# Kernel optimization log

Measured on AMD Instinct MI355X. Metric: run time of the kernel, lower is better.

Reference implementation:

```python
import jax, jax.numpy as jnp
import numpy as np

B, S, E, H = 2, 2048, 1024, 16
D = E // H  # head_dim = 64


def setup_inputs() -> dict:
    key = jax.random.key(0)
    ks = jax.random.split(key, 8)
    s = 0.02
    return {
        "queries": jax.random.normal(ks[0], (B, S, E), jnp.float32),
        "keys": jax.random.normal(ks[1], (B, S, E), jnp.float32),
        "values": jax.random.normal(ks[2], (B, S, E), jnp.float32),
        "mask": jnp.ones((B, 1, 1, S), jnp.int32),
        "Wq": jax.random.normal(ks[3], (E, E), jnp.float32) * s,
        "bq": jnp.zeros((E,), jnp.float32),
        "Wk": jax.random.normal(ks[4], (E, E), jnp.float32) * s,
        "bk": jnp.zeros((E,), jnp.float32),
        "Wv": jax.random.normal(ks[5], (E, E), jnp.float32) * s,
        "bv": jnp.zeros((E,), jnp.float32),
        "Wo": jax.random.normal(ks[6], (E, E), jnp.float32) * s,
        "bo": jnp.zeros((E,), jnp.float32),
    }


def reference(queries, keys, values, mask, Wq, bq, Wk, bk, Wv, bv, Wo, bo):
    # NOTE: faithful to source, W_v is applied to the `keys` input; `values` is unused.
    q = queries @ Wq.T + bq            # [B,S,E]
    k = keys @ Wk.T + bk               # [B,S,E]
    v = keys @ Wv.T + bv               # [B,S,E]
    q = q.reshape(B, S, H, D)
    k = k.reshape(B, S, H, D)
    v = v.reshape(B, S, H, D)
    scale = 1.0 / jnp.sqrt(jnp.asarray(D, q.dtype))
    scores = jnp.einsum("nqhd,nkhd->nhqk", q, k)   # [B,H,S,S] full score matrix
    scores = jnp.where(mask == 0, jnp.asarray(-1e20, scores.dtype), scores)
    attn = jax.nn.softmax(scores * scale, axis=-1)
    out = jnp.einsum("nhqk,nkhd->nqhd", attn, v).reshape(B, S, E)
    return out @ Wo.T + bo
```

## Files before the change

### kernel.cpp

```cpp
#include <hip/hip_runtime.h>
#include <hip/hip_bf16.h>
#include <stdint.h>

#define NB 2
#define NS 2048
#define NE 1024
#define NH 16
#define ND 64

typedef __attribute__((ext_vector_type(4))) float f32x4;
typedef __attribute__((ext_vector_type(16))) float f32x16;
typedef __attribute__((ext_vector_type(8))) short s16x8;
typedef __attribute__((ext_vector_type(4))) unsigned short u16x4;
typedef __attribute__((ext_vector_type(2))) unsigned int uint2v;

__device__ __forceinline__ unsigned short f2bf(float f) {
  union { float f; unsigned int i; } u; u.f = f;
  unsigned int r = u.i + 0x7FFFu + ((u.i >> 16) & 1u);
  return (unsigned short)(r >> 16);
}

__device__ __forceinline__ unsigned cvtpk_bf16(float lo, float hi) {
  unsigned r;
  asm("v_cvt_pk_bf16_f32 %0, %1, %2" : "=v"(r) : "v"(lo), "v"(hi));
  return r;
}

__device__ __forceinline__ void gload_lds16(const void* g, void* l) {
  __builtin_amdgcn_global_load_lds(
      (const __attribute__((address_space(1))) uint32_t*)g,
      (__attribute__((address_space(3))) uint32_t*)l, 16, 0, 0);
}

__device__ __forceinline__ f32x4 mfma16(s16x8 a, s16x8 b, f32x4 c) {
  return __builtin_amdgcn_mfma_f32_16x16x32_bf16(a, b, c, 0, 0, 0);
}
__device__ __forceinline__ f32x16 mfma32(s16x8 a, s16x8 b, f32x16 c) {
  return __builtin_amdgcn_mfma_f32_32x32x16_bf16(a, b, c, 0, 0, 0);
}

__global__ void conv_x2(const float* __restrict__ a, const float* __restrict__ b,
                        unsigned short* __restrict__ da, unsigned short* __restrict__ db,
                        int n4) {
  const float* s = blockIdx.y ? b : a;
  unsigned short* d = blockIdx.y ? db : da;
  int i = blockIdx.x * blockDim.x + threadIdx.x;
  int stride = gridDim.x * blockDim.x;
  for (; i < n4; i += stride) {
    float4 v = ((const float4*)s)[i];
    u16x4 o;
    o.x = f2bf(v.x); o.y = f2bf(v.y); o.z = f2bf(v.z); o.w = f2bf(v.w);
    ((u16x4*)d)[i] = o;
  }
}

__global__ void conv_w4(const float* __restrict__ s0, const float* __restrict__ s1,
                        const float* __restrict__ s2, const float* __restrict__ s3,
                        unsigned short* __restrict__ d0, unsigned short* __restrict__ d1,
                        unsigned short* __restrict__ d2, unsigned short* __restrict__ d3,
                        int n4) {
  const float* s; unsigned short* d;
  switch (blockIdx.y) {
    case 0: s = s0; d = d0; break;
    case 1: s = s1; d = d1; break;
    case 2: s = s2; d = d2; break;
    default: s = s3; d = d3; break;
  }
  int i = blockIdx.x * blockDim.x + threadIdx.x;
  int stride = gridDim.x * blockDim.x;
  for (; i < n4; i += stride) {
    float4 v = ((const float4*)s)[i];
    u16x4 o;
    o.x = f2bf(v.x); o.y = f2bf(v.y); o.z = f2bf(v.z); o.w = f2bf(v.w);
    ((u16x4*)d)[i] = o;
  }
}

template <int EPI>
__global__ __launch_bounds__(256, 2) void gemm_bt(
    const unsigned short* __restrict__ A,
    const unsigned short* __restrict__ W0, const unsigned short* __restrict__ W1,
    const float* __restrict__ b0, const float* __restrict__ b1,
    void* __restrict__ out0, void* __restrict__ out1) {
  constexpr int BM = 64;
  constexpr int K = 1024;
  __shared__ char smem[2 * (BM * 128 + 16384)];
  const int t = threadIdx.x;
  const int lane = t & 63;
  const int wv = t >> 6;
  const int wr = wv >> 1, wc = wv & 1;
  const int bm = blockIdx.y * BM, bn = blockIdx.x * 128;
  const int lr = lane & 15, lg = lane >> 4;

  const unsigned short* Wp = W0;
  const float* bp = b0;
  int nloc = bn;
  if constexpr (EPI == 3) {
    if (bn >= 1024) { Wp = W1; bp = b1; nloc = bn - 1024; }
  }

  f32x4 acc[2][4] = {};

  auto stage = [&](int buf, int k0) {
    char* As = smem + buf * (BM * 128 + 16384);
    char* Bs = As + BM * 128;
#pragma unroll
    for (int r = 0; r < BM / 32; ++r) {
      int lin = r * 256 + t;
      int row = lin >> 3;
      int scb = ((lin & 7) << 4) ^ ((row & 7) << 4);
      gload_lds16((const char*)(A + (size_t)(bm + row) * K + k0) + scb,
                  As + (size_t)(r * 256 + (t & ~63)) * 16);
    }
#pragma unroll
    for (int r = 0; r < 4; ++r) {
      int lin = r * 256 + t;
      int row = lin >> 3;
      int scb = ((lin & 7) << 4) ^ ((row & 7) << 4);
      gload_lds16((const char*)(Wp + (size_t)(nloc + row) * K + k0) + scb,
                  Bs + (size_t)(r * 256 + (t & ~63)) * 16);
    }
  };

  stage(0, 0);
  for (int t6 = 0; t6 < K / 64; ++t6) {
    const int cur = t6 & 1;
    if (t6 + 1 < K / 64) {
      stage(cur ^ 1, (t6 + 1) * 64);
      asm volatile("s_waitcnt vmcnt(6)" ::: "memory");
    } else {
      asm volatile("s_waitcnt vmcnt(0)" ::: "memory");
    }
    asm volatile("s_barrier" ::: "memory");

    const char* As = smem + cur * (BM * 128 + 16384);
    const char* Bs = As + BM * 128;
    s16x8 af[2][2], bfr[4][2];
#pragma unroll
    for (int mf = 0; mf < 2; ++mf)
#pragma unroll
      for (int kk = 0; kk < 2; ++kk) {
        int row = wr * 32 + mf * 16 + lr;
        int cb = (lg << 4) + (kk << 6);
        af[mf][kk] = *(const s16x8*)(As + row * 128 + (cb ^ ((row & 7) << 4)));
      }
#pragma unroll
    for (int nf = 0; nf < 4; ++nf)
#pragma unroll
      for (int kk = 0; kk < 2; ++kk) {
        int row = wc * 64 + nf * 16 + lr;
        int cb = (lg << 4) + (kk << 6);
        bfr[nf][kk] = *(const s16x8*)(Bs + row * 128 + (cb ^ ((row & 7) << 4)));
      }
#pragma unroll
    for (int mf = 0; mf < 2; ++mf)
#pragma unroll
      for (int nf = 0; nf < 4; ++nf)
#pragma unroll
        for (int kk = 0; kk < 2; ++kk)
          acc[mf][nf] = mfma16(af[mf][kk], bfr[nf][kk], acc[mf][nf]);

    asm volatile("s_waitcnt lgkmcnt(0)" ::: "memory");
    asm volatile("s_barrier" ::: "memory");
  }

#pragma unroll
  for (int mf = 0; mf < 2; ++mf)
#pragma unroll
    for (int nf = 0; nf < 4; ++nf) {
      int m0 = bm + wr * 32 + mf * 16 + (lg << 2);
      int nc = wc * 64 + nf * 16 + lr;
      int n = bn + nc;
      float bv = bp[nloc + nc];
      if constexpr (EPI == 0) {
        unsigned short* C = (unsigned short*)out0;
#pragma unroll
        for (int r = 0; r < 4; ++r)
          C[(size_t)(m0 + r) * 1024 + n] = f2bf(acc[mf][nf][r] + bv);
      } else if constexpr (EPI == 2) {
        float* C = (float*)out0;
#pragma unroll
        for (int r = 0; r < 4; ++r)
          C[(size_t)(m0 + r) * 1024 + n] = acc[mf][nf][r] + bv;
      } else {
        if (n < 1024) {
          unsigned short* C = (unsigned short*)out0;
#pragma unroll
          for (int r = 0; r < 4; ++r)
            C[(size_t)(m0 + r) * 1024 + n] = f2bf(acc[mf][nf][r] + bv);
        } else {
          unsigned short* C = (unsigned short*)out1;
          int nv = n - 1024;
          int b = m0 >> 11, s = m0 & 2047;
          u16x4 o;
          o.x = f2bf(acc[mf][nf][0] + bv);
          o.y = f2bf(acc[mf][nf][1] + bv);
          o.z = f2bf(acc[mf][nf][2] + bv);
          o.w = f2bf(acc[mf][nf][3] + bv);
          *(u16x4*)&C[((size_t)b * NE + nv) * NS + s] = o;
        }
      }
    }
}

__global__ __launch_bounds__(256, 2) void attn_fwd(
    const unsigned short* __restrict__ qb, const unsigned short* __restrict__ kb,
    const unsigned short* __restrict__ vt, const int* __restrict__ mask,
    unsigned short* __restrict__ ob) {
  __shared__ char smem[32768];
  const int t = threadIdx.x, lane = t & 63, wv = t >> 6;
  const int l31 = lane & 31, hi = lane >> 5;
  const int sw = (l31 & 15) << 4;
  const int bh = blockIdx.y, b = bh >> 4, h = bh & 15;
  const int q = blockIdx.x * 128 + wv * 32 + l31;
  const float C = 0.18033688f;

  s16x8 qf[4];
#pragma unroll
  for (int ks = 0; ks < 4; ++ks)
    qf[ks] = *(const s16x8*)&qb[((size_t)(b * NS + q)) * NE + h * ND + ks * 16 + hi * 8];

  f32x16 oacc[2] = {};
  float m = -1e30f, l = 0.f;

  auto stage = [&](int buf, int kt) {
    char* Ks = smem + buf * 16384;
    char* Vs = Ks + 8192;
#pragma unroll
    for (int r = 0; r < 2; ++r) {
      int L = (r * 256 + t) * 16;
      int row = L >> 8;
      int offp = (L & 255) ^ ((row & 15) << 4);
      int key = row + ((offp >> 7) << 5);
      int dby = offp & 127;
      gload_lds16((const char*)&kb[((size_t)(b * NS + kt + key)) * NE + h * ND] + dby,
                  Ks + (r * 256 + (t & ~63)) * 16);
    }
#pragma unroll
    for (int r = 0; r < 2; ++r) {
      int L = (r * 256 + t) * 16;
      int row = L >> 8;
      int offp = (L & 255) ^ ((row & 15) << 4);
      int d = row + ((offp >> 7) << 5);
      int kby = offp & 127;
      gload_lds16((const char*)&vt[((size_t)((b * NH + h) * ND + d)) * NS + kt] + kby,
                  Vs + (r * 256 + (t & ~63)) * 16);
    }
  };

  stage(0, 0);
  asm volatile("s_waitcnt vmcnt(0)" ::: "memory");
  __syncthreads();

  for (int kt = 0; kt < NS; kt += 64) {
    const int cur = (kt >> 6) & 1;
    if (kt + 64 < NS) stage(cur ^ 1, kt + 64);
    const char* Ks = smem + cur * 16384;
    const char* Vs = Ks + 8192;

    int mk = mask[b * NS + kt + lane];

    f32x16 st[2] = {};
    __builtin_amdgcn_s_setprio(1);
#pragma unroll
    for (int t2 = 0; t2 < 2; ++t2)
#pragma unroll
      for (int ks = 0; ks < 4; ++ks) {
        s16x8 kf = *(const s16x8*)(Ks + l31 * 256 +
                                   ((t2 * 128 + ks * 32 + hi * 16) ^ sw));
        st[t2] = mfma32(kf, qf[ks], st[t2]);
      }
    __builtin_amdgcn_s_setprio(0);

    float tm[16];
#pragma unroll
    for (int r = 0; r < 16; ++r) tm[r] = fmaxf(st[0][r], st[1][r]);
    float a0 = fmaxf(fmaxf(tm[0], tm[1]), tm[2]);
    float a1 = fmaxf(fmaxf(tm[3], tm[4]), tm[5]);
    float a2 = fmaxf(fmaxf(tm[6], tm[7]), tm[8]);
    float a3 = fmaxf(fmaxf(tm[9], tm[10]), tm[11]);
    float a4 = fmaxf(fmaxf(tm[12], tm[13]), tm[14]);
    float b0 = fmaxf(fmaxf(a0, a1), a2);
    float b1 = fmaxf(fmaxf(a3, a4), tm[15]);
    float mxl = fmaxf(b0, b1);
    float mx = fmaxf(mxl, __shfl_xor(mxl, 32));

    if (!__all(mx - m <= 44.0f)) {
      float mnew = fmaxf(m, mx);
      float corr = __builtin_amdgcn_exp2f((m - mnew) * C);
#pragma unroll
      for (int td = 0; td < 2; ++td)
#pragma unroll
        for (int r = 0; r < 16; ++r) oacc[td][r] *= corr;
      l *= corr;
      m = mnew;
    }
    const float mC = m * C;

#pragma unroll
    for (int t2 = 0; t2 < 2; ++t2)
#pragma unroll
      for (int r = 0; r < 16; ++r)
        st[t2][r] = __builtin_amdgcn_exp2f(__builtin_fmaf(st[t2][r], C, -mC));

    unsigned long long bal = __ballot(mk != 0);
    if (bal != ~0ull) {
#pragma unroll
      for (int t2 = 0; t2 < 2; ++t2)
#pragma unroll
        for (int r = 0; r < 16; ++r) {
          int key = t2 * 32 + (r & 3) + 8 * (r >> 2) + 4 * hi;
          if (!((bal >> key) & 1)) st[t2][r] = 0.f;
        }
    }

    float ps[16];
#pragma unroll
    for (int r = 0; r < 16; ++r) ps[r] = st[0][r] + st[1][r];
#pragma unroll
    for (int s = 8; s > 0; s >>= 1)
#pragma unroll
      for (int r = 0; r < s; ++r) ps[r] += ps[r + s];
    l += ps[0] + __shfl_xor(ps[0], 32);

    s16x8 pf[4];
#pragma unroll
    for (int ks = 0; ks < 4; ++ks) {
      const int t2 = ks >> 1, r0 = (ks & 1) * 8;
      unsigned wreg[4];
#pragma unroll
      for (int w = 0; w < 2; ++w) {
        unsigned x = cvtpk_bf16(st[t2][r0 + 2 * w], st[t2][r0 + 2 * w + 1]);
        unsigned y = cvtpk_bf16(st[t2][r0 + 4 + 2 * w], st[t2][r0 + 4 + 2 * w + 1]);
        uint2v r2 = __builtin_amdgcn_permlane32_swap(x, y, false, false);
        wreg[w] = r2.x;
        wreg[w + 2] = r2.y;
      }
      union { unsigned u[4]; s16x8 v; } pu;
      pu.u[0] = wreg[0]; pu.u[1] = wreg[1]; pu.u[2] = wreg[2]; pu.u[3] = wreg[3];
      pf[ks] = pu.v;
    }

    __builtin_amdgcn_s_setprio(1);
#pragma unroll
    for (int td = 0; td < 2; ++td)
#pragma unroll
      for (int ks = 0; ks < 4; ++ks) {
        s16x8 vf = *(const s16x8*)(Vs + l31 * 256 +
                                   ((td * 128 + ks * 32 + hi * 16) ^ sw));
        oacc[td] = mfma32(vf, pf[ks], oacc[td]);
      }
    __builtin_amdgcn_s_setprio(0);

    asm volatile("s_waitcnt vmcnt(0)" ::: "memory");
    __syncthreads();
  }

  float inv = 1.0f / l;
  char* Ob = smem + wv * 4096;
#pragma unroll
  for (int td = 0; td < 2; ++td)
#pragma unroll
    for (int i = 0; i < 8; ++i) {
      int r = 2 * i;
      int d = td * 32 + (r & 3) + 8 * (r >> 2) + 4 * hi;
      unsigned pk = cvtpk_bf16(oacc[td][r] * inv, oacc[td][r + 1] * inv);
      *(unsigned*)(Ob + l31 * 128 + ((d * 2) ^ ((l31 & 7) << 4))) = pk;
    }
#pragma unroll
  for (int p4 = 0; p4 < 4; ++p4) {
    int lq = p4 * 8 + (lane >> 3);
    int col = (lane & 7) * 16;
    s16x8 v0 = *(const s16x8*)(Ob + lq * 128 + (col ^ ((lq & 7) << 4)));
    int qg = blockIdx.x * 128 + wv * 32 + lq;
    *(s16x8*)((char*)&ob[((size_t)(b * NS + qg)) * NE + h * ND] + col) = v0;
  }
}

extern "C" void kernel_launch(void* const* d_in, const int* in_sizes, int n_in,
                              void* d_out, int out_size, void* d_ws, size_t ws_size,
                              hipStream_t stream) {
  const float* queries = (const float*)d_in[0];
  const float* keys = (const float*)d_in[1];
  const int* mask = (const int*)d_in[3];
  const float* Wq = (const float*)d_in[4];
  const float* bq = (const float*)d_in[5];
  const float* Wk = (const float*)d_in[6];
  const float* bk = (const float*)d_in[7];
  const float* Wv = (const float*)d_in[8];
  const float* bv = (const float*)d_in[9];
  const float* Wo = (const float*)d_in[10];
  const float* bo = (const float*)d_in[11];
  float* out = (float*)d_out;

  char* ws = (char*)d_ws;
  const size_t SZ_X = (size_t)NB * NS * NE * 2;
  const size_t SZ_W = (size_t)NE * NE * 2;
  unsigned short* qbf = (unsigned short*)(ws);
  unsigned short* kbf = (unsigned short*)(ws + SZ_X);
  unsigned short* wqb = (unsigned short*)(ws + 2 * SZ_X);
  unsigned short* wkb = (unsigned short*)(ws + 2 * SZ_X + SZ_W);
  unsigned short* wvb = (unsigned short*)(ws + 2 * SZ_X + 2 * SZ_W);
  unsigned short* wob = (unsigned short*)(ws + 2 * SZ_X + 3 * SZ_W);
  unsigned short* qp  = (unsigned short*)(ws + 2 * SZ_X + 4 * SZ_W);
  unsigned short* kp  = (unsigned short*)(ws + 3 * SZ_X + 4 * SZ_W);
  unsigned short* vtp = (unsigned short*)(ws + 4 * SZ_X + 4 * SZ_W);
  unsigned short* ao  = (unsigned short*)(ws + 5 * SZ_X + 4 * SZ_W);

  int nX4 = NB * NS * NE / 4, nW4 = NE * NE / 4;
  conv_x2<<<dim3(1024, 2), 256, 0, stream>>>(queries, keys, qbf, kbf, nX4);
  conv_w4<<<dim3(256, 4), 256, 0, stream>>>(Wq, Wk, Wv, Wo, wqb, wkb, wvb, wob, nW4);

  gemm_bt<0><<<dim3(8, 64), 256, 0, stream>>>(qbf, wqb, nullptr, bq, nullptr, qp, nullptr);
  gemm_bt<3><<<dim3(16, 64), 256, 0, stream>>>(kbf, wkb, wvb, bk, bv, kp, vtp);

  dim3 ga(NS / 128, NB * NH);
  attn_fwd<<<ga, 256, 0, stream>>>(qp, kp, vtp, mask, ao);

  gemm_bt<2><<<dim3(8, 64), 256, 0, stream>>>(ao, wob, nullptr, bo, nullptr, out, nullptr);
}
```

Before: 125.7 us.

## Merge QKV projections into one launch, prepack mask bits, triple-buffer attention loads

Merges the Q and K/V projection GEMMs into a single 24-column grid launch and raises the GEMM occupancy hint to 3 blocks per CU. Adds a mask_pack kernel that ballots the int mask into 64-bit words, so attention reads one word per tile via readlane instead of loading the mask on every iteration. The attention kernel now keeps two tiles in flight across four LDS buffers (64 KB), precomputes its load addresses and LDS offsets, and uses partial vmcnt waits with a single barrier per tile instead of waiting for all loads. The larger LDS footprint may cut attention occupancy, and the extra launch adds a small fixed cost.

Measured after the change: 119.4 us. 1.05x faster.

```diff
diff --git a/kernel.cpp b/kernel.cpp
--- a/kernel.cpp
+++ b/kernel.cpp
@@ -7,6 +7,7 @@
 #define NE 1024
 #define NH 16
 #define ND 64
+#define NT 32
 
 typedef __attribute__((ext_vector_type(4))) float f32x4;
 typedef __attribute__((ext_vector_type(16))) float f32x16;
@@ -76,28 +77,36 @@
   }
 }
 
-template <int EPI>
-__global__ __launch_bounds__(256, 2) void gemm_bt(
-    const unsigned short* __restrict__ A,
-    const unsigned short* __restrict__ W0, const unsigned short* __restrict__ W1,
-    const float* __restrict__ b0, const float* __restrict__ b1,
-    void* __restrict__ out0, void* __restrict__ out1) {
-  constexpr int BM = 64;
-  constexpr int K = 1024;
+__global__ void mask_pack(const int* __restrict__ mask, unsigned long long* __restrict__ bm) {
+  int w = blockIdx.x;
+  int lane = threadIdx.x;
+  int mk = mask[w * 64 + lane];
+  unsigned long long bal = __ballot(mk != 0);
+  if (lane == 0) bm[w] = bal;
+}
+
+__global__ __launch_bounds__(256, 3) void gemm_qkv(
+    const unsigned short* __restrict__ Aq, const unsigned short* __restrict__ Akv,
+    const unsigned short* __restrict__ Wqp, const unsigned short* __restrict__ Wkp,
+    const unsigned short* __restrict__ Wvp,
+    const float* __restrict__ bqp, const float* __restrict__ bkp, const float* __restrict__ bvp,
+    unsigned short* __restrict__ outq, unsigned short* __restrict__ outk,
+    unsigned short* __restrict__ outvt) {
+  constexpr int BM = 64, K = 1024;
   __shared__ char smem[2 * (BM * 128 + 16384)];
   const int t = threadIdx.x;
   const int lane = t & 63;
   const int wv = t >> 6;
   const int wr = wv >> 1, wc = wv & 1;
-  const int bm = blockIdx.y * BM, bn = blockIdx.x * 128;
+  const int x = blockIdx.x;
+  const int bm = blockIdx.y * BM;
   const int lr = lane & 15, lg = lane >> 4;
 
-  const unsigned short* Wp = W0;
-  const float* bp = b0;
-  int nloc = bn;
-  if constexpr (EPI == 3) {
-    if (bn >= 1024) { Wp = W1; bp = b1; nloc = bn - 1024; }
-  }
+  const unsigned short* A; const unsigned short* Wp; const float* bp;
+  unsigned short* outp; int nloc, mode;
+  if (x < 8)       { A = Aq;  Wp = Wqp; bp = bqp; outp = outq;  nloc = x * 128;        mode = 0; }
+  else if (x < 16) { A = Akv; Wp = Wkp; bp = bkp; outp = outk;  nloc = (x - 8) * 128;  mode = 0; }
+  else             { A = Akv; Wp = Wvp; bp = bvp; outp = outvt; nloc = (x - 16) * 128; mode = 1; }
 
   f32x4 acc[2][4] = {};
 
@@ -105,7 +114,7 @@
     char* As = smem + buf * (BM * 128 + 16384);
     char* Bs = As + BM * 128;
 #pragma unroll
-    for (int r = 0; r < BM / 32; ++r) {
+    for (int r = 0; r < 2; ++r) {
       int lin = r * 256 + t;
       int row = lin >> 3;
       int scb = ((lin & 7) << 4) ^ ((row & 7) << 4);
@@ -170,44 +179,118 @@
     for (int nf = 0; nf < 4; ++nf) {
       int m0 = bm + wr * 32 + mf * 16 + (lg << 2);
       int nc = wc * 64 + nf * 16 + lr;
-      int n = bn + nc;
       float bv = bp[nloc + nc];
-      if constexpr (EPI == 0) {
-        unsigned short* C = (unsigned short*)out0;
+      if (mode == 0) {
 #pragma unroll
         for (int r = 0; r < 4; ++r)
-          C[(size_t)(m0 + r) * 1024 + n] = f2bf(acc[mf][nf][r] + bv);
-      } else if constexpr (EPI == 2) {
-        float* C = (float*)out0;
-#pragma unroll
-        for (int r = 0; r < 4; ++r)
-          C[(size_t)(m0 + r) * 1024 + n] = acc[mf][nf][r] + bv;
+          outp[(size_t)(m0 + r) * 1024 + nloc + nc] = f2bf(acc[mf][nf][r] + bv);
       } else {
-        if (n < 1024) {
-          unsigned short* C = (unsigned short*)out0;
-#pragma unroll
-          for (int r = 0; r < 4; ++r)
-            C[(size_t)(m0 + r) * 1024 + n] = f2bf(acc[mf][nf][r] + bv);
-        } else {
-          unsigned short* C = (unsigned short*)out1;
-          int nv = n - 1024;
-          int b = m0 >> 11, s = m0 & 2047;
-          u16x4 o;
-          o.x = f2bf(acc[mf][nf][0] + bv);
-          o.y = f2bf(acc[mf][nf][1] + bv);
-          o.z = f2bf(acc[mf][nf][2] + bv);
-          o.w = f2bf(acc[mf][nf][3] + bv);
-          *(u16x4*)&C[((size_t)b * NE + nv) * NS + s] = o;
-        }
-      }
+        int b = m0 >> 11, s = m0 & 2047;
+        u16x4 o;
+        o.x = f2bf(acc[mf][nf][0] + bv);
+        o.y = f2bf(acc[mf][nf][1] + bv);
+        o.z = f2bf(acc[mf][nf][2] + bv);
+        o.w = f2bf(acc[mf][nf][3] + bv);
+        *(u16x4*)&outp[((size_t)b * NE + nloc + nc) * NS + s] = o;
+      }
+    }
+}
+
+__global__ __launch_bounds__(256, 3) void gemm_o(
+    const unsigned short* __restrict__ A, const unsigned short* __restrict__ W,
+    const float* __restrict__ bias, float* __restrict__ out) {
+  constexpr int BM = 64, K = 1024;
+  __shared__ char smem[2 * (BM * 128 + 16384)];
+  const int t = threadIdx.x;
+  const int lane = t & 63;
+  const int wv = t >> 6;
+  const int wr = wv >> 1, wc = wv & 1;
+  const int bm = blockIdx.y * BM, bn = blockIdx.x * 128;
+  const int lr = lane & 15, lg = lane >> 4;
+
+  f32x4 acc[2][4] = {};
+
+  auto stage = [&](int buf, int k0) {
+    char* As = smem + buf * (BM * 128 + 16384);
+    char* Bs = As + BM * 128;
+#pragma unroll
+    for (int r = 0; r < 2; ++r) {
+      int lin = r * 256 + t;
+      int row = lin >> 3;
+      int scb = ((lin & 7) << 4) ^ ((row & 7) << 4);
+      gload_lds16((const char*)(A + (size_t)(bm + row) * K + k0) + scb,
+                  As + (size_t)(r * 256 + (t & ~63)) * 16);
+    }
+#pragma unroll
+    for (int r = 0; r < 4; ++r) {
+      int lin = r * 256 + t;
+      int row = lin >> 3;
+      int scb = ((lin & 7) << 4) ^ ((row & 7) << 4);
+      gload_lds16((const char*)(W + (size_t)(bn + row) * K + k0) + scb,
+                  Bs + (size_t)(r * 256 + (t & ~63)) * 16);
+    }
+  };
+
+  stage(0, 0);
+  for (int t6 = 0; t6 < K / 64; ++t6) {
+    const int cur = t6 & 1;
+    if (t6 + 1 < K / 64) {
+      stage(cur ^ 1, (t6 + 1) * 64);
+      asm volatile("s_waitcnt vmcnt(6)" ::: "memory");
+    } else {
+      asm volatile("s_waitcnt vmcnt(0)" ::: "memory");
+    }
+    asm volatile("s_barrier" ::: "memory");
+
+    const char* As = smem + cur * (BM * 128 + 16384);
+    const char* Bs = As + BM * 128;
+    s16x8 af[2][2], bfr[4][2];
+#pragma unroll
+    for (int mf = 0; mf < 2; ++mf)
+#pragma unroll
+      for (int kk = 0; kk < 2; ++kk) {
+        int row = wr * 32 + mf * 16 + lr;
+        int cb = (lg << 4) + (kk << 6);
+        af[mf][kk] = *(const s16x8*)(As + row * 128 + (cb ^ ((row & 7) << 4)));
+      }
+#pragma unroll
+    for (int nf = 0; nf < 4; ++nf)
+#pragma unroll
+      for (int kk = 0; kk < 2; ++kk) {
+        int row = wc * 64 + nf * 16 + lr;
+        int cb = (lg << 4) + (kk << 6);
+        bfr[nf][kk] = *(const s16x8*)(Bs + row * 128 + (cb ^ ((row & 7) << 4)));
+      }
+#pragma unroll
+    for (int mf = 0; mf < 2; ++mf)
+#pragma unroll
+      for (int nf = 0; nf < 4; ++nf)
+#pragma unroll
+        for (int kk = 0; kk < 2; ++kk)
+          acc[mf][nf] = mfma16(af[mf][kk], bfr[nf][kk], acc[mf][nf]);
+
+    asm volatile("s_waitcnt lgkmcnt(0)" ::: "memory");
+    asm volatile("s_barrier" ::: "memory");
+  }
+
+#pragma unroll
+  for (int mf = 0; mf < 2; ++mf)
+#pragma unroll
+    for (int nf = 0; nf < 4; ++nf) {
+      int m0 = bm + wr * 32 + mf * 16 + (lg << 2);
+      int n = bn + wc * 64 + nf * 16 + lr;
+      float bv = bias[n];
+#pragma unroll
+      for (int r = 0; r < 4; ++r)
+        out[(size_t)(m0 + r) * 1024 + n] = acc[mf][nf][r] + bv;
     }
 }
 
 __global__ __launch_bounds__(256, 2) void attn_fwd(
     const unsigned short* __restrict__ qb, const unsigned short* __restrict__ kb,
-    const unsigned short* __restrict__ vt, const int* __restrict__ mask,
+    const unsigned short* __restrict__ vt, const unsigned long long* __restrict__ bmw,
     unsigned short* __restrict__ ob) {
-  __shared__ char smem[32768];
+  __shared__ char smem[65536];
   const int t = threadIdx.x, lane = t & 63, wv = t >> 6;
   const int l31 = lane & 31, hi = lane >> 5;
   const int sw = (l31 & 15) << 4;
@@ -220,45 +303,59 @@
   for (int ks = 0; ks < 4; ++ks)
     qf[ks] = *(const s16x8*)&qb[((size_t)(b * NS + q)) * NE + h * ND + ks * 16 + hi * 8];
 
+  unsigned long long mword = bmw[(size_t)b * 32 + l31];
+  unsigned mlo = (unsigned)mword, mhi = (unsigned)(mword >> 32);
+
+  const char* kSrc[2]; const char* vSrc[2]; int ldsK[2], ldsV[2];
+#pragma unroll
+  for (int r = 0; r < 2; ++r) {
+    int L = (r * 256 + t) * 16;
+    int row = L >> 8;
+    int offp = (L & 255) ^ ((row & 15) << 4);
+    int rr = row + ((offp >> 7) << 5);
+    int byo = offp & 127;
+    kSrc[r] = (const char*)&kb[((size_t)(b * NS) + rr) * NE + h * ND] + byo;
+    vSrc[r] = (const char*)&vt[((size_t)((b * NH + h) * ND) + rr) * NS] + byo;
+    ldsK[r] = (r * 256 + (t & ~63)) * 16;
+    ldsV[r] = 8192 + ldsK[r];
+  }
+
+  int off16[8];
+#pragma unroll
+  for (int j = 0; j < 8; ++j)
+    off16[j] = l31 * 256 + ((j * 32 + hi * 16) ^ sw);
+
+  auto stage = [&](int buf, int kt) {
+    char* base = smem + buf * 16384;
+#pragma unroll
+    for (int r = 0; r < 2; ++r)
+      gload_lds16(kSrc[r] + (size_t)kt * (NE * 2), base + ldsK[r]);
+#pragma unroll
+    for (int r = 0; r < 2; ++r)
+      gload_lds16(vSrc[r] + (size_t)kt * 2, base + ldsV[r]);
+  };
+
   f32x16 oacc[2] = {};
   float m = -1e30f, l = 0.f;
 
-  auto stage = [&](int buf, int kt) {
-    char* Ks = smem + buf * 16384;
-    char* Vs = Ks + 8192;
-#pragma unroll
-    for (int r = 0; r < 2; ++r) {
-      int L = (r * 256 + t) * 16;
-      int row = L >> 8;
-      int offp = (L & 255) ^ ((row & 15) << 4);
-      int key = row + ((offp >> 7) << 5);
-      int dby = offp & 127;
-      gload_lds16((const char*)&kb[((size_t)(b * NS + kt + key)) * NE + h * ND] + dby,
-                  Ks + (r * 256 + (t & ~63)) * 16);
-    }
-#pragma unroll
-    for (int r = 0; r < 2; ++r) {
-      int L = (r * 256 + t) * 16;
-      int row = L >> 8;
-      int offp = (L & 255) ^ ((row & 15) << 4);
-      int d = row + ((offp >> 7) << 5);
-      int kby = offp & 127;
-      gload_lds16((const char*)&vt[((size_t)((b * NH + h) * ND + d)) * NS + kt] + kby,
-                  Vs + (r * 256 + (t & ~63)) * 16);
-    }
-  };
-
   stage(0, 0);
+  stage(1, 64);
   asm volatile("s_waitcnt vmcnt(0)" ::: "memory");
   __syncthreads();
 
-  for (int kt = 0; kt < NS; kt += 64) {
-    const int cur = (kt >> 6) & 1;
-    if (kt + 64 < NS) stage(cur ^ 1, kt + 64);
-    const char* Ks = smem + cur * 16384;
+  auto body = [&](int tt, int buf) {
+    if (tt + 2 < NT) {
+      stage((buf + 2) & 3, (tt + 2) * 64);
+      asm volatile("s_waitcnt vmcnt(8)" ::: "memory");
+    } else if (tt + 1 < NT) {
+      asm volatile("s_waitcnt vmcnt(4)" ::: "memory");
+    } else {
+      asm volatile("s_waitcnt vmcnt(0)" ::: "memory");
+    }
+    __builtin_amdgcn_s_barrier();
+
+    const char* Ks = smem + buf * 16384;
     const char* Vs = Ks + 8192;
-
-    int mk = mask[b * NS + kt + lane];
 
     f32x16 st[2] = {};
     __builtin_amdgcn_s_setprio(1);
@@ -266,8 +363,7 @@
     for (int t2 = 0; t2 < 2; ++t2)
 #pragma unroll
       for (int ks = 0; ks < 4; ++ks) {
-        s16x8 kf = *(const s16x8*)(Ks + l31 * 256 +
-                                   ((t2 * 128 + ks * 32 + hi * 16) ^ sw));
+        s16x8 kf = *(const s16x8*)(Ks + off16[t2 * 4 + ks]);
         st[t2] = mfma32(kf, qf[ks], st[t2]);
       }
     __builtin_amdgcn_s_setprio(0);
@@ -303,7 +399,9 @@
       for (int r = 0; r < 16; ++r)
         st[t2][r] = __builtin_amdgcn_exp2f(__builtin_fmaf(st[t2][r], C, -mC));
 
-    unsigned long long bal = __ballot(mk != 0);
+    unsigned lo = (unsigned)__builtin_amdgcn_readlane((int)mlo, tt);
+    unsigned hh = (unsigned)__builtin_amdgcn_readlane((int)mhi, tt);
+    unsigned long long bal = ((unsigned long long)hh << 32) | lo;
     if (bal != ~0ull) {
 #pragma unroll
       for (int t2 = 0; t2 < 2; ++t2)
@@ -346,14 +444,17 @@
     for (int td = 0; td < 2; ++td)
 #pragma unroll
       for (int ks = 0; ks < 4; ++ks) {
-        s16x8 vf = *(const s16x8*)(Vs + l31 * 256 +
-                                   ((td * 128 + ks * 32 + hi * 16) ^ sw));
+        s16x8 vf = *(const s16x8*)(Vs + off16[td * 4 + ks]);
         oacc[td] = mfma32(vf, pf[ks], oacc[td]);
       }
     __builtin_amdgcn_s_setprio(0);
-
-    asm volatile("s_waitcnt vmcnt(0)" ::: "memory");
-    __syncthreads();
+  };
+
+  for (int tt = 0; tt < NT; tt += 4) {
+    body(tt + 0, 0);
+    body(tt + 1, 1);
+    body(tt + 2, 2);
+    body(tt + 3, 3);
   }
 
   float inv = 1.0f / l;
@@ -406,16 +507,18 @@
   unsigned short* kp  = (unsigned short*)(ws + 3 * SZ_X + 4 * SZ_W);
   unsigned short* vtp = (unsigned short*)(ws + 4 * SZ_X + 4 * SZ_W);
   unsigned short* ao  = (unsigned short*)(ws + 5 * SZ_X + 4 * SZ_W);
+  unsigned long long* bmp = (unsigned long long*)(ws + 6 * SZ_X + 4 * SZ_W);
 
   int nX4 = NB * NS * NE / 4, nW4 = NE * NE / 4;
   conv_x2<<<dim3(1024, 2), 256, 0, stream>>>(queries, keys, qbf, kbf, nX4);
   conv_w4<<<dim3(256, 4), 256, 0, stream>>>(Wq, Wk, Wv, Wo, wqb, wkb, wvb, wob, nW4);
-
-  gemm_bt<0><<<dim3(8, 64), 256, 0, stream>>>(qbf, wqb, nullptr, bq, nullptr, qp, nullptr);
-  gemm_bt<3><<<dim3(16, 64), 256, 0, stream>>>(kbf, wkb, wvb, bk, bv, kp, vtp);
+  mask_pack<<<NB * NS / 64, 64, 0, stream>>>(mask, bmp);
+
+  gemm_qkv<<<dim3(24, 64), 256, 0, stream>>>(qbf, kbf, wqb, wkb, wvb,
+                                             bq, bk, bv, qp, kp, vtp);
 
   dim3 ga(NS / 128, NB * NH);
-  attn_fwd<<<ga, 256, 0, stream>>>(qp, kp, vtp, mask, ao);
-
-  gemm_bt<2><<<dim3(8, 64), 256, 0, stream>>>(ao, wob, nullptr, bo, nullptr, out, nullptr);
-}
+  attn_fwd<<<ga, 256, 0, stream>>>(qp, kp, vtp, bmp, ao);
+
+  gemm_o<<<dim3(8, 64), 256, 0, stream>>>(ao, wob, bo, out);
+}
```
